# Performance work log

Measured on AMD Instinct MI355X. Metric: run time of the kernel, lower is better.

## Reference

```python
import jax, jax.numpy as jnp
import numpy as np

B, T = 64, 512
VOCAB, E, H = 20, 64, 128
D = 2 * H            # 256, bidirectional LSTM output dim
NH, KD = 8, D // 8   # 8 heads, key_dim 32
DU, OUT = 256, 128
NEG = -1e9


def _lstm_scan(x, mask, W, U, b):
    # x: [B,T,E], mask: [B,T] bool. Keras gate order: i, f, g(c), o.
    Bb = x.shape[0]
    Hh = U.shape[0]
    def step(carry, inp):
        h, c = carry
        xt, mt = inp                      # [B,E], [B]
        z = xt @ W + h @ U + b            # [B,4H]
        i, f, g, o = jnp.split(z, 4, axis=-1)
        c_new = jax.nn.sigmoid(f) * c + jax.nn.sigmoid(i) * jnp.tanh(g)
        h_new = jax.nn.sigmoid(o) * jnp.tanh(c_new)
        m = mt[:, None]
        h = jnp.where(m, h_new, h)        # freeze state/output on masked steps
        c = jnp.where(m, c_new, c)
        return (h, c), h
    h0 = jnp.zeros((Bb, Hh), x.dtype)
    _, ys = jax.lax.scan(step, (h0, h0), (jnp.swapaxes(x, 0, 1), mask.T))
    return jnp.swapaxes(ys, 0, 1)         # [B,T,H]


def setup_inputs() -> dict:
    key = jax.random.key(0)
    ks = jax.random.split(key, 24)
    g = lambda k, shape, s: (jax.random.normal(k, shape, jnp.float32) * s)
    inp = {
        'sequences': jax.random.randint(ks[0], (B, T), 0, VOCAB),
        'emb': g(ks[1], (VOCAB, E), 0.05),
        # forward LSTM
        'Wf': g(ks[2], (E, 4 * H), 0.05), 'Uf': g(ks[3], (H, 4 * H), 0.05), 'bf': jnp.zeros((4 * H,), jnp.float32),
        # backward LSTM
        'Wb': g(ks[4], (E, 4 * H), 0.05), 'Ub': g(ks[5], (H, 4 * H), 0.05), 'bb': jnp.zeros((4 * H,), jnp.float32),
        # MHA projections
        'Wq': g(ks[6], (D, NH, KD), 0.05), 'bq': jnp.zeros((NH, KD), jnp.float32),
        'Wk': g(ks[7], (D, NH, KD), 0.05), 'bk': jnp.zeros((NH, KD), jnp.float32),
        'Wv': g(ks[8], (D, NH, KD), 0.05), 'bv': jnp.zeros((NH, KD), jnp.float32),
        'Wo': g(ks[9], (NH, KD, D), 0.05), 'bo': jnp.zeros((D,), jnp.float32),
        # MLP head (input is concat of avg+max pool -> 2*D)
        'W1': g(ks[10], (2 * D, DU), 0.05), 'b1': jnp.zeros((DU,), jnp.float32),
        'W2': g(ks[11], (DU, DU // 2), 0.05), 'b2': jnp.zeros((DU // 2,), jnp.float32),
        'W3': g(ks[12], (DU // 2, OUT), 0.05), 'b3': jnp.zeros((OUT,), jnp.float32),
    }
    return inp


def _forward(sequences, emb, Wf, Uf, bf, Wb, Ub, bb, Wq, bq, Wk, bk, Wv, bv, Wo, bo, W1, b1, W2, b2, W3, b3):
    mask = sequences != 0                       # mask_zero=True
    x = emb[sequences]                          # [B,T,E]
    fwd = _lstm_scan(x, mask, Wf, Uf, bf)
    bwd = _lstm_scan(x[:, ::-1], mask[:, ::-1], Wb, Ub, bb)[:, ::-1]
    h = jnp.concatenate([fwd, bwd], axis=-1)    # [B,T,D]
    # Multi-head self-attention (key-masked, Keras MHA math)
    q = jnp.einsum('btd,dhk->bthk', h, Wq) + bq
    k = jnp.einsum('btd,dhk->bthk', h, Wk) + bk
    v = jnp.einsum('btd,dhk->bthk', h, Wv) + bv
    scores = jnp.einsum('bthk,bshk->bhts', q, k) / jnp.sqrt(jnp.float32(KD))
    scores = jnp.where(mask[:, None, None, :], scores, NEG)
    attn = jax.nn.softmax(scores, axis=-1)      # [B,H,T,T]
    ctx = jnp.einsum('bhts,bshk->bthk', attn, v)
    att = jnp.einsum('bthk,hkd->btd', ctx, Wo) + bo   # [B,T,D]
    # dual pooling (masked mean + masked max)
    mf = mask[..., None].astype(att.dtype)
    avg = (att * mf).sum(axis=1) / jnp.maximum(mf.sum(axis=1), 1.0)
    mx = jnp.where(mask[..., None], att, NEG).max(axis=1)
    p = jnp.concatenate([avg, mx], axis=-1)     # [B,2D]
    x1 = jax.nn.relu(p @ W1 + b1)
    x2 = jax.nn.relu(x1 @ W2 + b2)
    return x2 @ W3 + b3                         # [B,OUT]


def reference(sequences, emb, Wf, Uf, bf, Wb, Ub, bb, Wq, bq, Wk, bk, Wv, bv, Wo, bo, W1, b1, W2, b2, W3, b3):
    return _forward(sequences, emb, Wf, Uf, bf, Wb, Ub, bb, Wq, bq, Wk, bk, Wv, bv, Wo, bo, W1, b1, W2, b2, W3, b3)
```

## Files before the change

kernel.cpp:

```cpp
#include <hip/hip_runtime.h>
#include <math.h>

#define B_ 64
#define T_ 512
#define E_ 64
#define H_ 128
#define NH_ 8
#define KD_ 32
#define BT_ (B_ * T_)
#define NEG_ -1e9f

typedef __attribute__((ext_vector_type(8))) short bf16x8_t;
typedef __attribute__((ext_vector_type(4))) float f32x4_t;
typedef unsigned short ushort_t;
typedef unsigned int uint_t;

__device__ __forceinline__ float sigmoidf_(float x) {
    return 1.f / (1.f + __expf(-x));
}
__device__ __forceinline__ float tanhf_(float x) {
    return 1.f - 2.f / (1.f + __expf(2.f * x));
}

__device__ __forceinline__ ushort_t bf16_rne(float x) {
    uint_t u = __float_as_uint(x);
    uint_t r = (u + 0x7FFFu + ((u >> 16) & 1u)) >> 16;
    return (ushort_t)r;
}
__device__ __forceinline__ float bf16_to_f(ushort_t h) {
    return __uint_as_float(((uint_t)h) << 16);
}
__device__ __forceinline__ void split_bf16(float x, ushort_t& h, ushort_t& l) {
    h = bf16_rne(x);
    l = bf16_rne(x - bf16_to_f(h));
}

__device__ __forceinline__ float qswap1(float x) {
    return __int_as_float(__builtin_amdgcn_mov_dpp(__float_as_int(x), 0xB1, 0xF, 0xF, true));
}
__device__ __forceinline__ float qswap2(float x) {
    return __int_as_float(__builtin_amdgcn_mov_dpp(__float_as_int(x), 0x4E, 0xF, 0xF, true));
}

__global__ void prep_kernel(
    const float* __restrict__ emb,
    const float* __restrict__ Wf, const float* __restrict__ bf,
    const float* __restrict__ Wb, const float* __restrict__ bb,
    const float* __restrict__ Wq, const float* __restrict__ Wk,
    const float* __restrict__ Wv, const float* __restrict__ Wo,
    const float* __restrict__ bq, const float* __restrict__ bk,
    const float* __restrict__ bv,
    ushort_t* __restrict__ wqkvh, ushort_t* __restrict__ wqkvl,
    ushort_t* __restrict__ woh, ushort_t* __restrict__ wol,
    float* __restrict__ embWf, float* __restrict__ embWb,
    float* __restrict__ qkvb)
{
    const int blk = blockIdx.x, tid = threadIdx.x;
    if (blk < 1024) {
        const int m = blk >> 8, k = blk & 255;
        const float* W = (m == 0) ? Wq : (m == 1) ? Wk : (m == 2) ? Wv : Wo;
        float v = W[k * 256 + tid];
        ushort_t h, l;
        split_bf16(v, h, l);
        if (m < 3) {
            wqkvh[(m * 256 + tid) * 256 + k] = h;
            wqkvl[(m * 256 + tid) * 256 + k] = l;
        } else {
            woh[tid * 256 + k] = h;
            wol[tid * 256 + k] = l;
        }
    } else if (blk < 1028) {
        const int e = blk - 1024;
        const int dir = e >> 1, half = e & 1;
        const float* W = dir ? Wb : Wf;
        const float* bias = dir ? bb : bf;
        float* dst = dir ? embWb : embWf;
        const int np = half * 256 + tid;
        const int gin = ((np & 3) << 7) + (np >> 2);
        for (int v = 0; v < 20; ++v) {
            float acc = bias[gin];
            for (int k = 0; k < 64; ++k)
                acc = fmaf(emb[v * 64 + k], W[k * 512 + gin], acc);
            dst[v * 512 + np] = acc;
        }
    } else {
        qkvb[tid] = bq[tid];
        qkvb[256 + tid] = bk[tid];
        qkvb[512 + tid] = bv[tid];
    }
}

__global__ __launch_bounds__(256, 2) void gemm_mfma3(
    const ushort_t* __restrict__ Ah, const ushort_t* __restrict__ Al,
    const ushort_t* __restrict__ Bh, const ushort_t* __restrict__ Bl,
    const float* __restrict__ bias, float* __restrict__ C,
    int M, int N)
{
    __shared__ __align__(16) ushort_t Alds[2][128 * 40];
    __shared__ __align__(16) ushort_t Blds[2][128 * 40];

    const int tid = threadIdx.x;
    const int ntn = N >> 7;
    const int bm = blockIdx.x / ntn, bn = blockIdx.x % ntn;
    const int m0 = bm << 7, n0 = bn << 7;

    const int w = tid >> 6;
    const int wr = w >> 1, wc = w & 1;
    const int lane = tid & 63;
    const int fr = lane & 15, kg = lane >> 4;

    const int sr = tid >> 1;
    const int sh = (tid & 1) << 4;

    f32x4_t acc[4][4];
#pragma unroll
    for (int i = 0; i < 4; ++i)
#pragma unroll
        for (int j = 0; j < 4; ++j) acc[i][j] = (f32x4_t){0.f, 0.f, 0.f, 0.f};

    for (int ks = 0; ks < 8; ++ks) {
        const int k0 = ks << 5;
        __syncthreads();
        {
            const size_t ga = (size_t)(m0 + sr) * 256 + k0 + sh;
            const size_t gb = (size_t)(n0 + sr) * 256 + k0 + sh;
            const int ld = sr * 40 + sh;
            const uint4* pah = (const uint4*)(Ah + ga);
            const uint4* pal = (const uint4*)(Al + ga);
            const uint4* pbh = (const uint4*)(Bh + gb);
            const uint4* pbl = (const uint4*)(Bl + gb);
            uint4* qah = (uint4*)&Alds[0][ld];
            uint4* qal = (uint4*)&Alds[1][ld];
            uint4* qbh = (uint4*)&Blds[0][ld];
            uint4* qbl = (uint4*)&Blds[1][ld];
            qah[0] = pah[0]; qah[1] = pah[1];
            qal[0] = pal[0]; qal[1] = pal[1];
            qbh[0] = pbh[0]; qbh[1] = pbh[1];
            qbl[0] = pbl[0]; qbl[1] = pbl[1];
        }
        __syncthreads();

        bf16x8_t ah[4], al[4], bh[4], bl[4];
#pragma unroll
        for (int i = 0; i < 4; ++i) {
            const int ra = (wr * 64 + i * 16 + fr) * 40 + kg * 8;
            const int rb = (wc * 64 + i * 16 + fr) * 40 + kg * 8;
            ah[i] = *(const bf16x8_t*)&Alds[0][ra];
            al[i] = *(const bf16x8_t*)&Alds[1][ra];
            bh[i] = *(const bf16x8_t*)&Blds[0][rb];
            bl[i] = *(const bf16x8_t*)&Blds[1][rb];
        }
#pragma unroll
        for (int i = 0; i < 4; ++i)
#pragma unroll
            for (int j = 0; j < 4; ++j) {
                acc[i][j] = __builtin_amdgcn_mfma_f32_16x16x32_bf16(
                    ah[i], bh[j], acc[i][j], 0, 0, 0);
                acc[i][j] = __builtin_amdgcn_mfma_f32_16x16x32_bf16(
                    ah[i], bl[j], acc[i][j], 0, 0, 0);
                acc[i][j] = __builtin_amdgcn_mfma_f32_16x16x32_bf16(
                    al[i], bh[j], acc[i][j], 0, 0, 0);
            }
    }

#pragma unroll
    for (int j = 0; j < 4; ++j) {
        const int col = n0 + wc * 64 + j * 16 + fr;
        const float bv = bias[col];
#pragma unroll
        for (int i = 0; i < 4; ++i) {
#pragma unroll
            for (int r = 0; r < 4; ++r) {
                const int row = m0 + wr * 64 + i * 16 + kg * 4 + r;
                C[(size_t)row * N + col] = acc[i][j][r] + bv;
            }
        }
    }
}

__global__ __launch_bounds__(512, 2) void lstm_scan(
    const int* __restrict__ seq,
    const float* __restrict__ embWf, const float* __restrict__ embWb,
    const float* __restrict__ Uf, const float* __restrict__ Ub,
    ushort_t* __restrict__ hch, ushort_t* __restrict__ hcl)
{
    const int w = blockIdx.x;
    const int dir = w & 1, b = w >> 1;
    const float* eW = dir ? embWb : embWf;
    const float* U  = dir ? Ub  : Uf;
    const int tid = threadIdx.x;
    const int jj = tid >> 2, ks = tid & 3;

    __shared__ __align__(16) float hbuf[2][4][36];
    __shared__ int tkl[T_];

    float u[4][32];
    __builtin_amdgcn_sched_barrier(0);
#pragma unroll
    for (int g = 0; g < 4; ++g)
#pragma unroll
        for (int kk = 0; kk < 32; ++kk) {
            const float* p = U + (size_t)(32 * ks + kk) * 512 + g * 128 + jj;
            asm volatile("global_load_dword %0, %1, off"
                         : "=v"(u[g][kk]) : "v"(p));
        }
    asm volatile("s_waitcnt vmcnt(0)" ::: "memory");
    __builtin_amdgcn_sched_barrier(0);

    tkl[tid] = seq[b * T_ + tid];
    if (tid < 2 * 4 * 36) ((float*)hbuf)[tid] = 0.f;

    float h_cur = 0.f, c_cur = 0.f;
    ushort_t* hoh = hch + (size_t)b * T_ * 256 + dir * 128;
    ushort_t* hol = hcl + (size_t)b * T_ * 256 + dir * 128;

    __syncthreads();

    int te = dir ? (T_ - 1) : 0;
    int tok = tkl[te];
    float4 xwv = *(const float4*)&eW[tok * 512 + jj * 4];

    int p = 0;
    for (int t = 0; t < T_; ++t) {
        const int te_n  = dir ? (te - 1) : (te + 1);
        const int te_pf = (t == T_ - 1) ? te : te_n;
        const int tok_n = tkl[te_pf];
        const float4 xw_n = *(const float4*)&eW[tok_n * 512 + jj * 4];

        float a0 = 0.f, a1 = 0.f, a2 = 0.f, a3 = 0.f;
        const float* hc = hbuf[p][ks];
#pragma unroll
        for (int c = 0; c < 8; ++c) {
            const float4 h4 = *(const float4*)&hc[c * 4];
            a0 = fmaf(h4.x, u[0][c*4+0], a0); a0 = fmaf(h4.y, u[0][c*4+1], a0);
            a0 = fmaf(h4.z, u[0][c*4+2], a0); a0 = fmaf(h4.w, u[0][c*4+3], a0);
            a1 = fmaf(h4.x, u[1][c*4+0], a1); a1 = fmaf(h4.y, u[1][c*4+1], a1);
            a1 = fmaf(h4.z, u[1][c*4+2], a1); a1 = fmaf(h4.w, u[1][c*4+3], a1);
            a2 = fmaf(h4.x, u[2][c*4+0], a2); a2 = fmaf(h4.y, u[2][c*4+1], a2);
            a2 = fmaf(h4.z, u[2][c*4+2], a2); a2 = fmaf(h4.w, u[2][c*4+3], a2);
            a3 = fmaf(h4.x, u[3][c*4+0], a3); a3 = fmaf(h4.y, u[3][c*4+1], a3);
            a3 = fmaf(h4.z, u[3][c*4+2], a3); a3 = fmaf(h4.w, u[3][c*4+3], a3);
        }
        a0 += qswap1(a0); a0 += qswap2(a0);
        a1 += qswap1(a1); a1 += qswap2(a1);
        a2 += qswap1(a2); a2 += qswap2(a2);
        a3 += qswap1(a3); a3 += qswap2(a3);

        const float zi = xwv.x + a0, zf = xwv.y + a1;
        const float zg = xwv.z + a2, zo = xwv.w + a3;
        const float cn = fmaf(sigmoidf_(zf), c_cur, sigmoidf_(zi) * tanhf_(zg));
        const float hn = sigmoidf_(zo) * tanhf_(cn);
        const bool mt = (tok != 0);
        const float hm = mt ? hn : h_cur;
        c_cur = mt ? cn : c_cur;
        h_cur = hm;

        if ((jj >> 5) == ks) hbuf[1 - p][ks][jj & 31] = hm;
        if (ks == 0) {
            ushort_t hh, hl;
            split_bf16(hm, hh, hl);
            hoh[(size_t)te * 256 + jj] = hh;
            hol[(size_t)te * 256 + jj] = hl;
        }
        asm volatile("s_waitcnt lgkmcnt(0)\n\ts_barrier" ::: "memory");
        p ^= 1; te = te_n; tok = tok_n; xwv = xw_n;
    }
}

__global__ __launch_bounds__(256, 2) void attn_fused(
    const int* __restrict__ seq,
    const float* __restrict__ qkv,
    ushort_t* __restrict__ cxh, ushort_t* __restrict__ cxl)
{
    const int wg = blockIdx.x;
    const int b = wg >> 3, h = wg & 7;
    const int tid = threadIdx.x;

    __shared__ __align__(16) float Ks[16][32];
    __shared__ __align__(16) float Vs[16][32];
    __shared__ float mk[16];

    float qA[32], qB[32];
    {
        const float* qp  = qkv + ((size_t)(b * T_) + tid) * 768 + h * KD_;
        const float* qp2 = qp + (size_t)256 * 768;
#pragma unroll
        for (int k = 0; k < 32; k += 4) {
            float4 v0 = *(const float4*)(qp + k);
            float4 v1 = *(const float4*)(qp2 + k);
            qA[k] = v0.x; qA[k + 1] = v0.y; qA[k + 2] = v0.z; qA[k + 3] = v0.w;
            qB[k] = v1.x; qB[k + 1] = v1.y; qB[k + 2] = v1.z; qB[k + 3] = v1.w;
        }
    }
    float ctxA[32], ctxB[32];
#pragma unroll
    for (int k = 0; k < 32; ++k) { ctxA[k] = 0.f; ctxB[k] = 0.f; }
    float mA = -1e30f, mB = -1e30f, lA = 0.f, lB = 0.f;

    const int lr = (tid & 127) >> 3;
    const int lc = (tid & 7) << 2;
    const bool loadV = (tid >= 128);

    for (int c = 0; c < T_ / 16; ++c) {
        const int s0 = c << 4;
        __syncthreads();
        {
            const float* src = qkv + ((size_t)(b * T_) + s0 + lr) * 768 +
                               (loadV ? 512 : 256) + h * KD_ + lc;
            float4 v = *(const float4*)src;
            if (loadV) *(float4*)&Vs[lr][lc] = v;
            else       *(float4*)&Ks[lr][lc] = v;
            if (tid < 16) mk[tid] = (seq[b * T_ + s0 + tid] != 0) ? 0.f : 1.f;
        }
        __syncthreads();

        float sA[16], sB[16];
#pragma unroll
        for (int s = 0; s < 16; ++s) {
            float dA = 0.f, dB = 0.f;
#pragma unroll
            for (int k = 0; k < 32; k += 4) {
                float4 k4 = *(const float4*)&Ks[s][k];
                dA = fmaf(k4.x, qA[k], dA); dA = fmaf(k4.y, qA[k + 1], dA);
                dA = fmaf(k4.z, qA[k + 2], dA); dA = fmaf(k4.w, qA[k + 3], dA);
                dB = fmaf(k4.x, qB[k], dB); dB = fmaf(k4.y, qB[k + 1], dB);
                dB = fmaf(k4.z, qB[k + 2], dB); dB = fmaf(k4.w, qB[k + 3], dB);
            }
            const float SCL = 0.17677669529663687f;
            const bool masked = (mk[s] > 0.5f);
            sA[s] = masked ? NEG_ : dA * SCL;
            sB[s] = masked ? NEG_ : dB * SCL;
        }
        float cmA = sA[0], cmB = sB[0];
#pragma unroll
        for (int s = 1; s < 16; ++s) {
            cmA = fmaxf(cmA, sA[s]); cmB = fmaxf(cmB, sB[s]);
        }
        const float mnA = fmaxf(mA, cmA), mnB = fmaxf(mB, cmB);
        const float alA = __expf(mA - mnA), alB = __expf(mB - mnB);
        float psA = 0.f, psB = 0.f;
#pragma unroll
        for (int s = 0; s < 16; ++s) {
            float pa = __expf(sA[s] - mnA); sA[s] = pa; psA += pa;
            float pb = __expf(sB[s] - mnB); sB[s] = pb; psB += pb;
        }
        lA = fmaf(lA, alA, psA); lB = fmaf(lB, alB, psB);
        mA = mnA; mB = mnB;
#pragma unroll
        for (int k = 0; k < 32; ++k) { ctxA[k] *= alA; ctxB[k] *= alB; }
#pragma unroll
        for (int s = 0; s < 16; ++s) {
#pragma unroll
            for (int k = 0; k < 32; k += 4) {
                float4 v4 = *(const float4*)&Vs[s][k];
                ctxA[k]     = fmaf(sA[s], v4.x, ctxA[k]);
                ctxA[k + 1] = fmaf(sA[s], v4.y, ctxA[k + 1]);
                ctxA[k + 2] = fmaf(sA[s], v4.z, ctxA[k + 2]);
                ctxA[k + 3] = fmaf(sA[s], v4.w, ctxA[k + 3]);
                ctxB[k]     = fmaf(sB[s], v4.x, ctxB[k]);
                ctxB[k + 1] = fmaf(sB[s], v4.y, ctxB[k + 1]);
                ctxB[k + 2] = fmaf(sB[s], v4.z, ctxB[k + 2]);
                ctxB[k + 3] = fmaf(sB[s], v4.w, ctxB[k + 3]);
            }
        }
    }

    const float iA = 1.f / lA, iB = 1.f / lB;
    ushort_t* chA = cxh + (((size_t)(b * T_) + tid) * NH_ + h) * KD_;
    ushort_t* clA = cxl + (((size_t)(b * T_) + tid) * NH_ + h) * KD_;
    ushort_t* chB = chA + (size_t)256 * NH_ * KD_;
    ushort_t* clB = clA + (size_t)256 * NH_ * KD_;
#pragma unroll
    for (int k = 0; k < 32; ++k) {
        ushort_t hA, lA_, hB, lB_;
        split_bf16(ctxA[k] * iA, hA, lA_);
        split_bf16(ctxB[k] * iB, hB, lB_);
        chA[k] = hA; clA[k] = lA_;
        chB[k] = hB; clB[k] = lB_;
    }
}

__global__ __launch_bounds__(256) void poolmlp_kernel(
    const int* __restrict__ seq, const float* __restrict__ att,
    const float* __restrict__ W1, const float* __restrict__ b1,
    const float* __restrict__ W2, const float* __restrict__ b2,
    const float* __restrict__ W3, const float* __restrict__ b3,
    float* __restrict__ out)
{
    const int b = blockIdx.x;
    const int tid = threadIdx.x;
    __shared__ float mk[T_];
    __shared__ float pl[512];
    __shared__ float x1l[256];
    __shared__ float x2l[128];

    for (int t = tid; t < T_; t += 256)
        mk[t] = (seq[b * T_ + t] != 0) ? 1.f : 0.f;
    __syncthreads();

    float sum = 0.f, mx = NEG_, cnt = 0.f;
    for (int t = 0; t < T_; ++t) {
        const float a = att[((size_t)b * T_ + t) * 256 + tid];
        const float m = mk[t];
        cnt += m;
        sum = fmaf(m, a, sum);
        mx = fmaxf(mx, (m > 0.5f) ? a : NEG_);
    }
    pl[tid] = sum / fmaxf(cnt, 1.f);
    pl[256 + tid] = mx;
    __syncthreads();

    {
        float acc = b1[tid];
        for (int k = 0; k < 512; ++k) acc = fmaf(pl[k], W1[k * 256 + tid], acc);
        x1l[tid] = fmaxf(acc, 0.f);
    }
    __syncthreads();
    if (tid < 128) {
        float acc = b2[tid];
        for (int k = 0; k < 256; ++k) acc = fmaf(x1l[k], W2[k * 128 + tid], acc);
        x2l[tid] = fmaxf(acc, 0.f);
    }
    __syncthreads();
    if (tid < 128) {
        float acc = b3[tid];
        for (int k = 0; k < 128; ++k) acc = fmaf(x2l[k], W3[k * 128 + tid], acc);
        out[b * 128 + tid] = acc;
    }
}

extern "C" void kernel_launch(void* const* d_in, const int* in_sizes, int n_in,
                              void* d_out, int out_size, void* d_ws, size_t ws_size,
                              hipStream_t stream)
{
    (void)in_sizes; (void)n_in; (void)out_size; (void)ws_size;
    const int*   seq = (const int*)d_in[0];
    const float* emb = (const float*)d_in[1];
    const float* Wf  = (const float*)d_in[2];
    const float* Uf  = (const float*)d_in[3];
    const float* bf  = (const float*)d_in[4];
    const float* Wb  = (const float*)d_in[5];
    const float* Ub  = (const float*)d_in[6];
    const float* bb  = (const float*)d_in[7];
    const float* Wq  = (const float*)d_in[8];
    const float* bq  = (const float*)d_in[9];
    const float* Wk  = (const float*)d_in[10];
    const float* bk  = (const float*)d_in[11];
    const float* Wv  = (const float*)d_in[12];
    const float* bv  = (const float*)d_in[13];
    const float* Wo  = (const float*)d_in[14];
    const float* bo  = (const float*)d_in[15];
    const float* W1  = (const float*)d_in[16];
    const float* b1  = (const float*)d_in[17];
    const float* W2  = (const float*)d_in[18];
    const float* b2  = (const float*)d_in[19];
    const float* W3  = (const float*)d_in[20];
    const float* b3  = (const float*)d_in[21];
    float* out = (float*)d_out;
    float* ws  = (float*)d_ws;

    float* qkv  = ws;
    ushort_t* cxh = (ushort_t*)(ws + 25165824);
    ushort_t* cxl = cxh + (size_t)BT_ * 256;
    ushort_t* hch = (ushort_t*)(ws + 33554432);
    ushort_t* hcl = hch + (size_t)BT_ * 256;
    float* attb = ws + 33554432;
    ushort_t* wt = (ushort_t*)(ws + 41943040);
    ushort_t* wqkvh = wt;
    ushort_t* wqkvl = wt + 196608;
    ushort_t* woh   = wt + 393216;
    ushort_t* wol   = wt + 458752;
    float* embWf = ws + 41943040 + 262144;
    float* embWb = embWf + 20 * 512;
    float* qkvb  = embWb + 20 * 512;

    const dim3 blk256(256);

    prep_kernel<<<dim3(1029), blk256, 0, stream>>>(
        emb, Wf, bf, Wb, bb, Wq, Wk, Wv, Wo, bq, bk, bv,
        wqkvh, wqkvl, woh, wol, embWf, embWb, qkvb);

    lstm_scan<<<dim3(128), dim3(512), 0, stream>>>(
        seq, embWf, embWb, Uf, Ub, hch, hcl);

    gemm_mfma3<<<dim3((BT_ / 128) * 6), blk256, 0, stream>>>(
        hch, hcl, wqkvh, wqkvl, qkvb, qkv, BT_, 768);

    attn_fused<<<dim3(B_ * NH_), blk256, 0, stream>>>(seq, qkv, cxh, cxl);

    gemm_mfma3<<<dim3((BT_ / 128) * 2), blk256, 0, stream>>>(
        cxh, cxl, woh, wol, bo, attb, BT_, 256);

    poolmlp_kernel<<<dim3(B_), blk256, 0, stream>>>(
        seq, attb, W1, b1, W2, b2, W3, b3, out);
}
```

Before: 931.2 us.

## Compute LSTM recurrent matvec with split-bf16 MFMA instead of scalar FMAs

Replaces the per-step scalar FMA recurrence (fp32 U held in registers, reduced across quad lanes with DPP) with 16x16x32 bf16 MFMA instructions. U is split into high and low bf16 parts and h is shared through LDS as high/low bf16, with three MFMAs per tile to approximate fp32 precision. The embedding-projection table layout is permuted so each wave's 16 lanes read its gate inputs directly. Only 16 of the 64 lanes per wave do the gate math, the MFMA's M dimension is mostly wasted on a single batch row, and the split-bf16 recurrence carries some precision risk.

```diff
diff --git a/kernel.cpp b/kernel.cpp
--- a/kernel.cpp
+++ b/kernel.cpp
@@ -33,13 +33,6 @@
 __device__ __forceinline__ void split_bf16(float x, ushort_t& h, ushort_t& l) {
     h = bf16_rne(x);
     l = bf16_rne(x - bf16_to_f(h));
-}
-
-__device__ __forceinline__ float qswap1(float x) {
-    return __int_as_float(__builtin_amdgcn_mov_dpp(__float_as_int(x), 0xB1, 0xF, 0xF, true));
-}
-__device__ __forceinline__ float qswap2(float x) {
-    return __int_as_float(__builtin_amdgcn_mov_dpp(__float_as_int(x), 0x4E, 0xF, 0xF, true));
 }
 
 __global__ void prep_kernel(
@@ -52,7 +45,7 @@
     const float* __restrict__ bv,
     ushort_t* __restrict__ wqkvh, ushort_t* __restrict__ wqkvl,
     ushort_t* __restrict__ woh, ushort_t* __restrict__ wol,
-    float* __restrict__ embWf, float* __restrict__ embWb,
+    float* __restrict__ eWpf, float* __restrict__ eWpb,
     float* __restrict__ qkvb)
 {
     const int blk = blockIdx.x, tid = threadIdx.x;
@@ -74,14 +67,16 @@
         const int dir = e >> 1, half = e & 1;
         const float* W = dir ? Wb : Wf;
         const float* bias = dir ? bb : bf;
-        float* dst = dir ? embWb : embWf;
-        const int np = half * 256 + tid;
-        const int gin = ((np & 3) << 7) + (np >> 2);
+        float* dst = dir ? eWpb : eWpf;
+        const int cp = half * 256 + tid;
+        const int wv = cp >> 6, rem = cp & 63;
+        const int g = rem >> 4, ul = rem & 15;
+        const int gin = g * 128 + wv * 16 + ul;
         for (int v = 0; v < 20; ++v) {
             float acc = bias[gin];
             for (int k = 0; k < 64; ++k)
                 acc = fmaf(emb[v * 64 + k], W[k * 512 + gin], acc);
-            dst[v * 512 + np] = acc;
+            dst[v * 512 + cp] = acc;
         }
     } else {
         qkvb[tid] = bq[tid];
@@ -180,90 +175,127 @@
 
 __global__ __launch_bounds__(512, 2) void lstm_scan(
     const int* __restrict__ seq,
-    const float* __restrict__ embWf, const float* __restrict__ embWb,
+    const float* __restrict__ eWpf, const float* __restrict__ eWpb,
     const float* __restrict__ Uf, const float* __restrict__ Ub,
     ushort_t* __restrict__ hch, ushort_t* __restrict__ hcl)
 {
     const int w = blockIdx.x;
     const int dir = w & 1, b = w >> 1;
-    const float* eW = dir ? embWb : embWf;
+    const float* eW = dir ? eWpb : eWpf;
     const float* U  = dir ? Ub  : Uf;
     const int tid = threadIdx.x;
-    const int jj = tid >> 2, ks = tid & 3;
-
-    __shared__ __align__(16) float hbuf[2][4][36];
+    const int wv = tid >> 6;
+    const int l  = tid & 63;
+    const int lr = l & 15;
+    const int kg = l >> 4;
+
+    __shared__ __align__(16) ushort_t hhs[2][128];
+    __shared__ __align__(16) ushort_t hls[2][128];
     __shared__ int tkl[T_];
 
-    float u[4][32];
-    __builtin_amdgcn_sched_barrier(0);
+    bf16x8_t ubh[4][4], ubl[4][4];
 #pragma unroll
     for (int g = 0; g < 4; ++g)
 #pragma unroll
-        for (int kk = 0; kk < 32; ++kk) {
-            const float* p = U + (size_t)(32 * ks + kk) * 512 + g * 128 + jj;
-            asm volatile("global_load_dword %0, %1, off"
-                         : "=v"(u[g][kk]) : "v"(p));
-        }
-    asm volatile("s_waitcnt vmcnt(0)" ::: "memory");
-    __builtin_amdgcn_sched_barrier(0);
+        for (int kc = 0; kc < 4; ++kc) {
+            short th[8], tl[8];
+#pragma unroll
+            for (int j = 0; j < 8; ++j) {
+                const float v =
+                    U[(size_t)(kc * 32 + kg * 8 + j) * 512 + g * 128 + wv * 16 + lr];
+                ushort_t hh_, ll_;
+                split_bf16(v, hh_, ll_);
+                th[j] = (short)hh_;
+                tl[j] = (short)ll_;
+            }
+            ubh[g][kc] = *(const bf16x8_t*)th;
+            ubl[g][kc] = *(const bf16x8_t*)tl;
+            asm volatile("" : "+v"(ubh[g][kc]), "+v"(ubl[g][kc]));
+        }
 
     tkl[tid] = seq[b * T_ + tid];
-    if (tid < 2 * 4 * 36) ((float*)hbuf)[tid] = 0.f;
+    if (tid < 128) {
+        hhs[0][tid] = 0; hhs[1][tid] = 0;
+        hls[0][tid] = 0; hls[1][tid] = 0;
+    }
 
     float h_cur = 0.f, c_cur = 0.f;
-    ushort_t* hoh = hch + (size_t)b * T_ * 256 + dir * 128;
-    ushort_t* hol = hcl + (size_t)b * T_ * 256 + dir * 128;
+    const int u = wv * 16 + l;
+    ushort_t* hoh = hch + (size_t)b * T_ * 256 + dir * 128 + u;
+    ushort_t* hol = hcl + (size_t)b * T_ * 256 + dir * 128 + u;
 
     __syncthreads();
 
     int te = dir ? (T_ - 1) : 0;
     int tok = tkl[te];
-    float4 xwv = *(const float4*)&eW[tok * 512 + jj * 4];
+    float x0 = 0.f, x1 = 0.f, x2 = 0.f, x3 = 0.f;
+    if (l < 16) {
+        const float* xp = eW + tok * 512 + wv * 64 + l;
+        x0 = xp[0]; x1 = xp[16]; x2 = xp[32]; x3 = xp[48];
+    }
 
     int p = 0;
     for (int t = 0; t < T_; ++t) {
         const int te_n  = dir ? (te - 1) : (te + 1);
         const int te_pf = (t == T_ - 1) ? te : te_n;
         const int tok_n = tkl[te_pf];
-        const float4 xw_n = *(const float4*)&eW[tok_n * 512 + jj * 4];
-
-        float a0 = 0.f, a1 = 0.f, a2 = 0.f, a3 = 0.f;
-        const float* hc = hbuf[p][ks];
-#pragma unroll
-        for (int c = 0; c < 8; ++c) {
-            const float4 h4 = *(const float4*)&hc[c * 4];
-            a0 = fmaf(h4.x, u[0][c*4+0], a0); a0 = fmaf(h4.y, u[0][c*4+1], a0);
-            a0 = fmaf(h4.z, u[0][c*4+2], a0); a0 = fmaf(h4.w, u[0][c*4+3], a0);
-            a1 = fmaf(h4.x, u[1][c*4+0], a1); a1 = fmaf(h4.y, u[1][c*4+1], a1);
-            a1 = fmaf(h4.z, u[1][c*4+2], a1); a1 = fmaf(h4.w, u[1][c*4+3], a1);
-            a2 = fmaf(h4.x, u[2][c*4+0], a2); a2 = fmaf(h4.y, u[2][c*4+1], a2);
-            a2 = fmaf(h4.z, u[2][c*4+2], a2); a2 = fmaf(h4.w, u[2][c*4+3], a2);
-            a3 = fmaf(h4.x, u[3][c*4+0], a3); a3 = fmaf(h4.y, u[3][c*4+1], a3);
-            a3 = fmaf(h4.z, u[3][c*4+2], a3); a3 = fmaf(h4.w, u[3][c*4+3], a3);
-        }
-        a0 += qswap1(a0); a0 += qswap2(a0);
-        a1 += qswap1(a1); a1 += qswap2(a1);
-        a2 += qswap1(a2); a2 += qswap2(a2);
-        a3 += qswap1(a3); a3 += qswap2(a3);
-
-        const float zi = xwv.x + a0, zf = xwv.y + a1;
-        const float zg = xwv.z + a2, zo = xwv.w + a3;
-        const float cn = fmaf(sigmoidf_(zf), c_cur, sigmoidf_(zi) * tanhf_(zg));
-        const float hn = sigmoidf_(zo) * tanhf_(cn);
-        const bool mt = (tok != 0);
-        const float hm = mt ? hn : h_cur;
-        c_cur = mt ? cn : c_cur;
-        h_cur = hm;
-
-        if ((jj >> 5) == ks) hbuf[1 - p][ks][jj & 31] = hm;
-        if (ks == 0) {
-            ushort_t hh, hl;
-            split_bf16(hm, hh, hl);
-            hoh[(size_t)te * 256 + jj] = hh;
-            hol[(size_t)te * 256 + jj] = hl;
+        float x0n = 0.f, x1n = 0.f, x2n = 0.f, x3n = 0.f;
+        if (l < 16) {
+            const float* xp = eW + tok_n * 512 + wv * 64 + l;
+            x0n = xp[0]; x1n = xp[16]; x2n = xp[32]; x3n = xp[48];
+        }
+
+        bf16x8_t ah0 = *(const bf16x8_t*)&hhs[p][0 * 32 + kg * 8];
+        bf16x8_t ah1 = *(const bf16x8_t*)&hhs[p][1 * 32 + kg * 8];
+        bf16x8_t ah2 = *(const bf16x8_t*)&hhs[p][2 * 32 + kg * 8];
+        bf16x8_t ah3 = *(const bf16x8_t*)&hhs[p][3 * 32 + kg * 8];
+        bf16x8_t al0 = *(const bf16x8_t*)&hls[p][0 * 32 + kg * 8];
+        bf16x8_t al1 = *(const bf16x8_t*)&hls[p][1 * 32 + kg * 8];
+        bf16x8_t al2 = *(const bf16x8_t*)&hls[p][2 * 32 + kg * 8];
+        bf16x8_t al3 = *(const bf16x8_t*)&hls[p][3 * 32 + kg * 8];
+
+        f32x4_t C0 = {0.f, 0.f, 0.f, 0.f};
+        f32x4_t C1 = {0.f, 0.f, 0.f, 0.f};
+        f32x4_t C2 = {0.f, 0.f, 0.f, 0.f};
+        f32x4_t C3 = {0.f, 0.f, 0.f, 0.f};
+#define STEP_KC(AH, AL, KC)                                                    \
+        C0 = __builtin_amdgcn_mfma_f32_16x16x32_bf16(AH, ubh[0][KC], C0, 0, 0, 0); \
+        C0 = __builtin_amdgcn_mfma_f32_16x16x32_bf16(AH, ubl[0][KC], C0, 0, 0, 0); \
+        C0 = __builtin_amdgcn_mfma_f32_16x16x32_bf16(AL, ubh[0][KC], C0, 0, 0, 0); \
+        C1 = __builtin_amdgcn_mfma_f32_16x16x32_bf16(AH, ubh[1][KC], C1, 0, 0, 0); \
+        C1 = __builtin_amdgcn_mfma_f32_16x16x32_bf16(AH, ubl[1][KC], C1, 0, 0, 0); \
+        C1 = __builtin_amdgcn_mfma_f32_16x16x32_bf16(AL, ubh[1][KC], C1, 0, 0, 0); \
+        C2 = __builtin_amdgcn_mfma_f32_16x16x32_bf16(AH, ubh[2][KC], C2, 0, 0, 0); \
+        C2 = __builtin_amdgcn_mfma_f32_16x16x32_bf16(AH, ubl[2][KC], C2, 0, 0, 0); \
+        C2 = __builtin_amdgcn_mfma_f32_16x16x32_bf16(AL, ubh[2][KC], C2, 0, 0, 0); \
+        C3 = __builtin_amdgcn_mfma_f32_16x16x32_bf16(AH, ubh[3][KC], C3, 0, 0, 0); \
+        C3 = __builtin_amdgcn_mfma_f32_16x16x32_bf16(AH, ubl[3][KC], C3, 0, 0, 0); \
+        C3 = __builtin_amdgcn_mfma_f32_16x16x32_bf16(AL, ubh[3][KC], C3, 0, 0, 0);
+        STEP_KC(ah0, al0, 0)
+        STEP_KC(ah1, al1, 1)
+        STEP_KC(ah2, al2, 2)
+        STEP_KC(ah3, al3, 3)
+#undef STEP_KC
+
+        if (l < 16) {
+            const float zi = x0 + C0[0], zf = x1 + C1[0];
+            const float zg = x2 + C2[0], zo = x3 + C3[0];
+            const float cn = fmaf(sigmoidf_(zf), c_cur, sigmoidf_(zi) * tanhf_(zg));
+            const float hn = sigmoidf_(zo) * tanhf_(cn);
+            const bool mt = (tok != 0);
+            const float hm = mt ? hn : h_cur;
+            c_cur = mt ? cn : c_cur;
+            h_cur = hm;
+            ushort_t sh_, sl_;
+            split_bf16(hm, sh_, sl_);
+            hhs[1 - p][u] = sh_;
+            hls[1 - p][u] = sl_;
+            hoh[(size_t)te * 256] = sh_;
+            hol[(size_t)te * 256] = sl_;
         }
         asm volatile("s_waitcnt lgkmcnt(0)\n\ts_barrier" ::: "memory");
-        p ^= 1; te = te_n; tok = tok_n; xwv = xw_n;
+        p ^= 1; te = te_n; tok = tok_n;
+        x0 = x0n; x1 = x1n; x2 = x2n; x3 = x3n;
     }
 }
 
@@ -470,18 +502,18 @@
     ushort_t* wqkvl = wt + 196608;
     ushort_t* woh   = wt + 393216;
     ushort_t* wol   = wt + 458752;
-    float* embWf = ws + 41943040 + 262144;
-    float* embWb = embWf + 20 * 512;
-    float* qkvb  = embWb + 20 * 512;
+    float* eWpf = ws + 41943040 + 262144;
+    float* eWpb = eWpf + 20 * 512;
+    float* qkvb  = eWpb + 20 * 512;
 
     const dim3 blk256(256);
 
     prep_kernel<<<dim3(1029), blk256, 0, stream>>>(
         emb, Wf, bf, Wb, bb, Wq, Wk, Wv, Wo, bq, bk, bv,
-        wqkvh, wqkvl, woh, wol, embWf, embWb, qkvb);
+        wqkvh, wqkvl, woh, wol, eWpf, eWpb, qkvb);
 
     lstm_scan<<<dim3(128), dim3(512), 0, stream>>>(
-        seq, embWf, embWb, Uf, Ub, hch, hcl);
+        seq, eWpf, eWpb, Uf, Ub, hch, hcl);
 
     gemm_mfma3<<<dim3((BT_ / 128) * 6), blk256, 0, stream>>>(
         hch, hcl, wqkvh, wqkvl, qkvb, qkv, BT_, 768);
```

Measured after the change: 1.099 ms. +18.1%, slower.
